# Kernel optimization log

Hardware: AMD Instinct MI355X
Metric: run time of the kernel (lower is better)

The kernel has to match this reference:

```python
import jax, jax.numpy as jnp
import numpy as np

B, H, W = 4, 496, 496
M = 8  # max vertices of a quad-quad convex intersection


def _corners(boxes):
    # boxes [..., 7] = (x, y, z, dx, dy, dz, heading) -> CCW BEV corners [..., 4, 2]
    x, y, dx, dy, r = boxes[..., 0], boxes[..., 1], boxes[..., 3], boxes[..., 4], boxes[..., 6]
    lx = jnp.array([0.5, -0.5, -0.5, 0.5], dtype=boxes.dtype) * dx[..., None]
    ly = jnp.array([0.5, 0.5, -0.5, -0.5], dtype=boxes.dtype) * dy[..., None]
    c, s = jnp.cos(r)[..., None], jnp.sin(r)[..., None]
    cx = x[..., None] + c * lx - s * ly
    cy = y[..., None] + s * lx + c * ly
    return jnp.stack([cx, cy], axis=-1)


def _clip(poly, cnt, a, b):
    # Clip padded CCW polygon (poly [M,2], cnt valid verts) by halfplane left of edge a->b.
    idx = jnp.arange(M)
    valid = idx < cnt
    nidx = jnp.where(idx + 1 >= cnt, 0, idx + 1)
    cur, nxt = poly, poly[nidx]
    ex, ey = b[0] - a[0], b[1] - a[1]
    dc = ex * (cur[:, 1] - a[1]) - ey * (cur[:, 0] - a[0])  # signed dist of cur
    dn = ex * (nxt[:, 1] - a[1]) - ey * (nxt[:, 0] - a[0])
    inc, inn = dc >= 0, dn >= 0
    keep = inc & valid                      # emit cur if inside
    crs = (inc != inn) & valid              # emit edge/line intersection if crossing
    den = dc - dn
    t = dc / jnp.where(jnp.abs(den) < 1e-9, 1.0, den)
    ip = cur + t[:, None] * (nxt - cur)
    c = keep.astype(jnp.int32) + crs.astype(jnp.int32)
    offs = jnp.cumsum(c) - c                # exclusive prefix sum -> output slots
    out = jnp.zeros_like(poly)
    out = out.at[jnp.where(keep, offs, M)].set(cur, mode='drop')
    out = out.at[jnp.where(crs, offs + keep.astype(jnp.int32), M)].set(ip, mode='drop')
    return out, jnp.sum(c)


def _inter_area(ca, cb):
    # Intersection area of two CCW quads (each [4,2]) via Sutherland-Hodgman.
    poly = jnp.zeros((M, 2), ca.dtype).at[:4].set(ca)
    cnt = jnp.int32(4)
    for i in range(4):
        poly, cnt = _clip(poly, cnt, cb[i], cb[(i + 1) % 4])
    idx = jnp.arange(M)
    valid = idx < cnt
    nidx = jnp.where(idx + 1 >= cnt, 0, idx + 1)
    nxt = poly[nidx]
    cr = poly[:, 0] * nxt[:, 1] - nxt[:, 0] * poly[:, 1]  # shoelace terms
    return 0.5 * jnp.abs(jnp.sum(jnp.where(valid, cr, 0.0)))


def _iou3d_aligned(boxes_a, boxes_b):
    # Element-wise (aligned) 3D oriented-box IoU. boxes [N,7] -> iou [N].
    inter_bev = jax.vmap(_inter_area)(_corners(boxes_a), _corners(boxes_b))
    za0, za1 = boxes_a[:, 2] - 0.5 * boxes_a[:, 5], boxes_a[:, 2] + 0.5 * boxes_a[:, 5]
    zb0, zb1 = boxes_b[:, 2] - 0.5 * boxes_b[:, 5], boxes_b[:, 2] + 0.5 * boxes_b[:, 5]
    zo = jnp.maximum(jnp.minimum(za1, zb1) - jnp.maximum(za0, zb0), 0.0)
    inter_vol = inter_bev * zo
    vol_a = boxes_a[:, 3] * boxes_a[:, 4] * boxes_a[:, 5]
    vol_b = boxes_b[:, 3] * boxes_b[:, 4] * boxes_b[:, 5]
    return inter_vol / (vol_a + vol_b - inter_vol + 1e-7)


def setup_inputs() -> dict:
    key = jax.random.key(0)
    kc, kd, kr, kn, km, kp, ki = jax.random.split(key, 7)
    center = jax.random.normal(kc, (B, H, W, 3), dtype=jnp.float32) * 2.0
    dims = jax.random.uniform(kd, (B, H, W, 3), minval=0.5, maxval=3.0, dtype=jnp.float32)
    heading = jax.random.uniform(kr, (B, H, W, 1), minval=-np.pi, maxval=np.pi, dtype=jnp.float32)
    box_gt = jnp.concatenate([center, dims, heading], axis=-1)  # [B,H,W,7]
    pred = box_gt + jax.random.normal(kn, box_gt.shape, dtype=jnp.float32) * 0.1
    pred = pred.at[..., 3:6].set(jnp.maximum(pred[..., 3:6], 0.2))  # keep dims positive
    box_pred = jnp.transpose(pred, (0, 3, 1, 2))  # [B,7,H,W]
    mask = jax.random.randint(km, (B, H, W), 0, 2, dtype=jnp.int32)
    iou_pred = jax.random.normal(kp, (B, H, W), dtype=jnp.float32) * 0.5
    ind = jax.random.randint(ki, (B, 128), 0, H * W, dtype=jnp.int32)  # unused by the layer
    return {"iou_pred": iou_pred, "mask": mask, "ind": ind, "box_pred": box_pred, "box_gt": box_gt}


def reference(iou_pred, mask, ind, box_pred, box_gt):
    pred = jnp.transpose(box_pred, (0, 2, 3, 1)).reshape(-1, 7)  # [N,7]
    gt = box_gt.reshape(-1, 7)
    target = 2.0 * _iou3d_aligned(pred, gt) - 1.0               # [N]
    m = mask.astype(jnp.float32).reshape(-1)
    loss = jnp.sum(m * jnp.abs(iou_pred.reshape(-1) - target))
    return loss / (jnp.sum(m) + 1e-4)
```

## Files before the change

### kernel.cpp

```cpp
#include <hip/hip_runtime.h>
#include <math.h>

#define B_   4
#define H_   496
#define W_   496
#define HW_  (H_ * W_)
#define N_   (B_ * HW_)
#define TPB  256
#define NPT  2
#define EPB  (TPB * NPT)
#define NBLK (N_ / EPB)

static_assert(N_ % EPB == 0, "no tail");

__device__ __forceinline__ float clip_sum(const float px[4], const float py[4],
                                          const float qx[4], const float qy[4]) {
    float ex[4], ey[4], c0[4];
#pragma unroll
    for (int i = 0; i < 4; ++i) {
        ex[i] = qx[(i + 1) & 3] - qx[i];
        ey[i] = qy[(i + 1) & 3] - qy[i];
        c0[i] = ex[i] * qy[i] - ey[i] * qx[i];
    }
    float F[4][4];
#pragma unroll
    for (int i = 0; i < 4; ++i)
#pragma unroll
        for (int k = 0; k < 4; ++k)
            F[i][k] = fmaf(ex[i], py[k], fmaf(-ey[i], px[k], -c0[i]));

    float s = 0.f;
#pragma unroll
    for (int k = 0; k < 4; ++k) {
        const int   k1 = (k + 1) & 3;
        const float ax = px[k], ay = py[k];
        const float dx = px[k1] - ax, dy = py[k1] - ay;
        float t0 = 0.f, t1 = 1.f;
#pragma unroll
        for (int i = 0; i < 4; ++i) {
            const float fa = F[i][k], fb = F[i][k1];
            const float df = fb - fa;
            const float tc = -fa * __builtin_amdgcn_rcpf(df);
            const float tl = __builtin_amdgcn_fmed3f(tc, 0.f, 1.f);
            t0 = fmaxf(t0, (df > 0.f) ? tl : 0.f);
            t1 = fminf(t1, (df < 0.f) ? tl : 1.f);
        }
        const float x0 = fmaf(t0, dx, ax), y0 = fmaf(t0, dy, ay);
        const float x1 = fmaf(t1, dx, ax), y1 = fmaf(t1, dy, ay);
        const float c  = fmaf(x0, y1, -x1 * y0);
        s += (t1 > t0) ? c : 0.f;
    }
    return s;
}

__device__ __forceinline__ void iou_elem(
    int n, const float* __restrict__ iou_pred, const int* __restrict__ mask,
    const float* __restrict__ box_pred, const float* __restrict__ sg7,
    float& num, float& den)
{
    const int b  = n / HW_;
    const int hw = n - b * HW_;

    const float* bp = box_pred + (size_t)b * 7 * HW_ + hw;
    const float pax = bp[0];
    const float pay = bp[1 * HW_];
    const float paz = bp[2 * HW_];
    const float pdx = bp[3 * HW_];
    const float pdy = bp[4 * HW_];
    const float pdz = bp[5 * HW_];
    const float pr  = bp[6 * HW_];

    const float gax = sg7[0], gay = sg7[1], gaz = sg7[2];
    const float gdx = sg7[3], gdy = sg7[4], gdz = sg7[5], gr = sg7[6];

    float sp, cp; __sincosf(pr, &sp, &cp);
    float sg, cg; __sincosf(gr, &sg, &cg);
    const float phx = 0.5f * pdx, phy = 0.5f * pdy;
    const float ghx = 0.5f * gdx, ghy = 0.5f * gdy;

    float px[4], py[4], qx[4], qy[4];
    px[0] = pax + cp * phx - sp * phy;  py[0] = pay + sp * phx + cp * phy;
    px[1] = pax - cp * phx - sp * phy;  py[1] = pay - sp * phx + cp * phy;
    px[2] = pax - cp * phx + sp * phy;  py[2] = pay - sp * phx - cp * phy;
    px[3] = pax + cp * phx + sp * phy;  py[3] = pay + sp * phx - cp * phy;
    qx[0] = gax + cg * ghx - sg * ghy;  qy[0] = gay + sg * ghx + cg * ghy;
    qx[1] = gax - cg * ghx - sg * ghy;  qy[1] = gay - sg * ghx + cg * ghy;
    qx[2] = gax - cg * ghx + sg * ghy;  qy[2] = gay - sg * ghx - cg * ghy;
    qx[3] = gax + cg * ghx + sg * ghy;  qy[3] = gay + sg * ghx - cg * ghy;

    const float inter_bev = 0.5f * (clip_sum(px, py, qx, qy) +
                                    clip_sum(qx, qy, px, py));

    const float za0 = paz - 0.5f * pdz, za1 = paz + 0.5f * pdz;
    const float zb0 = gaz - 0.5f * gdz, zb1 = gaz + 0.5f * gdz;
    const float zo  = fmaxf(fminf(za1, zb1) - fmaxf(za0, zb0), 0.f);
    const float iv  = inter_bev * zo;
    const float va  = pdx * pdy * pdz;
    const float vb  = gdx * gdy * gdz;
    const float iou = iv / (va + vb - iv + 1e-7f);
    const float target = 2.f * iou - 1.f;

    const float m = (float)mask[n];
    num += m * fabsf(iou_pred[n] - target);
    den += m;
}

__global__ __launch_bounds__(TPB) void iou_main(
    const float* __restrict__ iou_pred,
    const int*   __restrict__ mask,
    const float* __restrict__ box_pred,
    const float* __restrict__ box_gt,
    float2* __restrict__ ws)
{
    __shared__ float sgt[EPB * 7];
    __shared__ float rn[4], rd[4];

    const int tid  = threadIdx.x;
    const int base = blockIdx.x * EPB;

    {
        const float4* g4 = (const float4*)(box_gt + (size_t)base * 7);
        float4* s4 = (float4*)sgt;
#pragma unroll
        for (int it = 0; it < (EPB * 7) / (4 * TPB); ++it)
            s4[tid + it * TPB] = g4[tid + it * TPB];
        const int idx = tid + 3 * TPB;
        if (idx < (EPB * 7) / 4) s4[idx] = g4[idx];
    }
    __syncthreads();

    float num = 0.f, den = 0.f;
#pragma unroll
    for (int e = 0; e < NPT; ++e) {
        const int n = base + e * TPB + tid;
        iou_elem(n, iou_pred, mask, box_pred, sgt + (e * TPB + tid) * 7, num, den);
    }

#pragma unroll
    for (int off = 32; off > 0; off >>= 1) {
        num += __shfl_down(num, off);
        den += __shfl_down(den, off);
    }
    if ((tid & 63) == 0) { rn[tid >> 6] = num; rd[tid >> 6] = den; }
    __syncthreads();
    if (tid == 0)
        ws[blockIdx.x] = make_float2(rn[0] + rn[1] + rn[2] + rn[3],
                                     rd[0] + rd[1] + rd[2] + rd[3]);
}

__global__ __launch_bounds__(TPB) void iou_fin(const float2* __restrict__ ws,
                                               float* __restrict__ out) {
    __shared__ float rn[4], rd[4];
    float sn = 0.f, sd = 0.f;
    for (int i = threadIdx.x; i < NBLK; i += TPB) {
        const float2 v = ws[i];
        sn += v.x;
        sd += v.y;
    }
#pragma unroll
    for (int off = 32; off > 0; off >>= 1) {
        sn += __shfl_down(sn, off);
        sd += __shfl_down(sd, off);
    }
    const int tid = threadIdx.x;
    if ((tid & 63) == 0) { rn[tid >> 6] = sn; rd[tid >> 6] = sd; }
    __syncthreads();
    if (tid == 0)
        out[0] = (rn[0] + rn[1] + rn[2] + rn[3]) /
                 (rd[0] + rd[1] + rd[2] + rd[3] + 1e-4f);
}

extern "C" void kernel_launch(void* const* d_in, const int* in_sizes, int n_in,
                              void* d_out, int out_size, void* d_ws, size_t ws_size,
                              hipStream_t stream) {
    const float* iou_pred = (const float*)d_in[0];
    const int*   mask     = (const int*)  d_in[1];
    const float* box_pred = (const float*)d_in[3];
    const float* box_gt   = (const float*)d_in[4];
    float*  out = (float*)d_out;
    float2* ws  = (float2*)d_ws;

    iou_main<<<NBLK, TPB, 0, stream>>>(iou_pred, mask, box_pred, box_gt, ws);
    iou_fin<<<1, TPB, 0, stream>>>(ws, out);
}
```

Measured before the change: 108.4 us.

## Compute BEV overlap in the GT box frame using axis-aligned edge clipping

Transforms the predicted box into the ground-truth box's local frame, so one polygon becomes an axis-aligned rectangle. Each edge is then clipped against four axis-aligned half-planes with precomputed reciprocals, and the shoelace contributions are computed in closed form. This replaces the general 4x4 edge-function matrix and the per-pair rcp calls in both clip directions, aiming to cut VALU work in this compute-bound kernel. The risk is numerical divergence in degenerate cases where an edge component is near zero and its reciprocal becomes inf.

```diff
diff --git a/kernel.cpp b/kernel.cpp
--- a/kernel.cpp
+++ b/kernel.cpp
@@ -13,44 +13,24 @@
 
 static_assert(N_ % EPB == 0, "no tail");
 
-__device__ __forceinline__ float clip_sum(const float px[4], const float py[4],
-                                          const float qx[4], const float qy[4]) {
-    float ex[4], ey[4], c0[4];
-#pragma unroll
-    for (int i = 0; i < 4; ++i) {
-        ex[i] = qx[(i + 1) & 3] - qx[i];
-        ey[i] = qy[(i + 1) & 3] - qy[i];
-        c0[i] = ex[i] * qy[i] - ey[i] * qx[i];
-    }
-    float F[4][4];
-#pragma unroll
-    for (int i = 0; i < 4; ++i)
-#pragma unroll
-        for (int k = 0; k < 4; ++k)
-            F[i][k] = fmaf(ex[i], py[k], fmaf(-ey[i], px[k], -c0[i]));
-
-    float s = 0.f;
-#pragma unroll
-    for (int k = 0; k < 4; ++k) {
-        const int   k1 = (k + 1) & 3;
-        const float ax = px[k], ay = py[k];
-        const float dx = px[k1] - ax, dy = py[k1] - ay;
-        float t0 = 0.f, t1 = 1.f;
-#pragma unroll
-        for (int i = 0; i < 4; ++i) {
-            const float fa = F[i][k], fb = F[i][k1];
-            const float df = fb - fa;
-            const float tc = -fa * __builtin_amdgcn_rcpf(df);
-            const float tl = __builtin_amdgcn_fmed3f(tc, 0.f, 1.f);
-            t0 = fmaxf(t0, (df > 0.f) ? tl : 0.f);
-            t1 = fminf(t1, (df < 0.f) ? tl : 1.f);
-        }
-        const float x0 = fmaf(t0, dx, ax), y0 = fmaf(t0, dy, ay);
-        const float x1 = fmaf(t1, dx, ax), y1 = fmaf(t1, dy, ay);
-        const float c  = fmaf(x0, y1, -x1 * y0);
-        s += (t1 > t0) ? c : 0.f;
-    }
-    return s;
+__device__ __forceinline__ float edge_delta(float xk, float yk,
+                                            float dx, float dy,
+                                            float rdx, float rdy,
+                                            float hx, float hy) {
+    float t0 = 0.f, t1 = 1.f, tl;
+    tl = __builtin_amdgcn_fmed3f((hy - yk) * rdy, 0.f, 1.f);
+    t0 = fmaxf(t0, (dy < 0.f) ? tl : 0.f);
+    t1 = fminf(t1, (dy > 0.f) ? tl : 1.f);
+    tl = __builtin_amdgcn_fmed3f(-(xk + hx) * rdx, 0.f, 1.f);
+    t0 = fmaxf(t0, (dx > 0.f) ? tl : 0.f);
+    t1 = fminf(t1, (dx < 0.f) ? tl : 1.f);
+    tl = __builtin_amdgcn_fmed3f(-(yk + hy) * rdy, 0.f, 1.f);
+    t0 = fmaxf(t0, (dy > 0.f) ? tl : 0.f);
+    t1 = fminf(t1, (dy < 0.f) ? tl : 1.f);
+    tl = __builtin_amdgcn_fmed3f((hx - xk) * rdx, 0.f, 1.f);
+    t0 = fmaxf(t0, (dx < 0.f) ? tl : 0.f);
+    t1 = fminf(t1, (dx > 0.f) ? tl : 1.f);
+    return fmaxf(t1 - t0, 0.f);
 }
 
 __device__ __forceinline__ void iou_elem(
@@ -75,26 +55,74 @@
 
     float sp, cp; __sincosf(pr, &sp, &cp);
     float sg, cg; __sincosf(gr, &sg, &cg);
+    const float cth = fmaf(cp, cg,  sp * sg);
+    const float sth = fmaf(sp, cg, -cp * sg);
+    const float wx = pax - gax, wy = pay - gay;
+    const float cx = fmaf(cg, wx,  sg * wy);
+    const float cy = fmaf(cg, wy, -sg * wx);
+
     const float phx = 0.5f * pdx, phy = 0.5f * pdy;
     const float ghx = 0.5f * gdx, ghy = 0.5f * gdy;
 
-    float px[4], py[4], qx[4], qy[4];
-    px[0] = pax + cp * phx - sp * phy;  py[0] = pay + sp * phx + cp * phy;
-    px[1] = pax - cp * phx - sp * phy;  py[1] = pay - sp * phx + cp * phy;
-    px[2] = pax - cp * phx + sp * phy;  py[2] = pay - sp * phx - cp * phy;
-    px[3] = pax + cp * phx + sp * phy;  py[3] = pay + sp * phx - cp * phy;
-    qx[0] = gax + cg * ghx - sg * ghy;  qy[0] = gay + sg * ghx + cg * ghy;
-    qx[1] = gax - cg * ghx - sg * ghy;  qy[1] = gay - sg * ghx + cg * ghy;
-    qx[2] = gax - cg * ghx + sg * ghy;  qy[2] = gay - sg * ghx - cg * ghy;
-    qx[3] = gax + cg * ghx + sg * ghy;  qy[3] = gay + sg * ghx - cg * ghy;
-
-    const float inter_bev = 0.5f * (clip_sum(px, py, qx, qy) +
-                                    clip_sum(qx, qy, px, py));
+    const float a1 = cth * phx, b1 = sth * phx;
+    const float a2 = sth * phy, b2 = cth * phy;
+    const float e1 = a1 - a2, e2 = a1 + a2;
+    const float f1 = b1 + b2, f2 = b1 - b2;
+    const float px0 = cx + e1, py0 = cy + f1;
+    const float px1 = cx - e2, py1 = cy - f2;
+    const float px2 = cx - e1, py2 = cy - f1;
+    const float px3 = cx + e2, py3 = cy + f2;
+
+    const float ta1 = a1 + a1, tb1 = b1 + b1;
+    const float ta2 = a2 + a2, tb2 = b2 + b2;
+    const float ra1 = __builtin_amdgcn_rcpf(ta1);
+    const float rb1 = __builtin_amdgcn_rcpf(tb1);
+    const float ra2 = __builtin_amdgcn_rcpf(ta2);
+    const float rb2 = __builtin_amdgcn_rcpf(tb2);
+
+    float inter;
+    {
+        const float d0 = edge_delta(px0, py0, -ta1, -tb1, -ra1, -rb1, ghx, ghy);
+        const float d1 = edge_delta(px1, py1,  ta2, -tb2,  ra2, -rb2, ghx, ghy);
+        const float d2 = edge_delta(px2, py2,  ta1,  tb1,  ra1,  rb1, ghx, ghy);
+        const float d3 = edge_delta(px3, py3, -ta2,  tb2, -ra2,  rb2, ghx, ghy);
+        inter =        d0 * fmaf(a1, py0, -b1 * px0);
+        inter = fmaf(  d1, -fmaf(b2, px1,  a2 * py1), inter);
+        inter = fmaf(  d2,  fmaf(b1, px2, -a1 * py2), inter);
+        inter = fmaf(  d3,  fmaf(b2, px3,  a2 * py3), inter);
+    }
+
+    {
+        const float A  = cth * ghx, Dv = sth * ghx;
+        const float Bq = sth * ghy, Ev = cth * ghy;
+        const float Cc = fmaf(cth, cx,  sth * cy);
+        const float Gf = fmaf(sth, cx, -cth * cy);
+        const float g1 = A + Bq,  g2 = A - Bq;
+        const float h1 = Ev - Dv, h2 = Ev + Dv;
+        const float u0 =  g1 - Cc, v0 =  h1 + Gf;
+        const float u1 = -g2 - Cc, v1 =  h2 + Gf;
+        const float u2 = -g1 - Cc, v2 = -h1 + Gf;
+        const float u3 =  g2 - Cc, v3 = -h2 + Gf;
+
+        const float tA = A + A,  tD = Dv + Dv;
+        const float tB = Bq + Bq, tE = Ev + Ev;
+        const float rA = __builtin_amdgcn_rcpf(tA);
+        const float rD = __builtin_amdgcn_rcpf(tD);
+        const float rB = __builtin_amdgcn_rcpf(tB);
+        const float rE = __builtin_amdgcn_rcpf(tE);
+
+        float sq;
+        sq  = edge_delta(u0, v0, -tA,  tD, -rA,  rD, phx, phy);
+        sq += edge_delta(u1, v1, -tB, -tE, -rB, -rE, phx, phy);
+        sq += edge_delta(u2, v2,  tA, -tD,  rA, -rD, phx, phy);
+        sq += edge_delta(u3, v3,  tB,  tE,  rB,  rE, phx, phy);
+        inter = fmaf(ghx * ghy, sq, inter);
+    }
 
     const float za0 = paz - 0.5f * pdz, za1 = paz + 0.5f * pdz;
     const float zb0 = gaz - 0.5f * gdz, zb1 = gaz + 0.5f * gdz;
     const float zo  = fmaxf(fminf(za1, zb1) - fmaxf(za0, zb0), 0.f);
-    const float iv  = inter_bev * zo;
+    const float iv  = inter * zo;
     const float va  = pdx * pdy * pdz;
     const float vb  = gdx * gdy * gdz;
     const float iou = iv / (va + vb - iv + 1e-7f);
@@ -122,7 +150,7 @@
         const float4* g4 = (const float4*)(box_gt + (size_t)base * 7);
         float4* s4 = (float4*)sgt;
 #pragma unroll
-        for (int it = 0; it < (EPB * 7) / (4 * TPB); ++it)
+        for (int it = 0; it < 3; ++it)
             s4[tid + it * TPB] = g4[tid + it * TPB];
         const int idx = tid + 3 * TPB;
         if (idx < (EPB * 7) / 4) s4[idx] = g4[idx];
```

Result: faster. 106.1 us (-2.1%).
